# Performance work log

Hardware: AMD Instinct MI355X
Metric: run time of the kernel (lower is better)

The kernel has to match this reference:

```python
import jax, jax.numpy as jnp
import numpy as np

GOLDEN_CENTER = 1.0 / np.e
GOLDEN_LOWER = 0.5 - np.log(4.0 / 3.0)
GOLDEN_UPPER = 0.5


def setup_inputs() -> dict:
    key = jax.random.key(0)
    ks = jax.random.split(key, 5)
    B, T, D, E, F = 2, 2048, 2048, 8, 2048  # F = intermediate_size // (E//2) = 8192//4
    s_in = 1.0 / np.sqrt(D)
    s_f = 1.0 / np.sqrt(F)
    return {
        "x": jax.random.normal(ks[0], (B, T, D), dtype=jnp.float32),
        "Wg": jax.random.normal(ks[1], (E, D, F), dtype=jnp.float32) * s_in,
        "Wu": jax.random.normal(ks[2], (E, D, F), dtype=jnp.float32) * s_in,
        "Wd": jax.random.normal(ks[3], (E, F, D), dtype=jnp.float32) * s_f,
        "Wr": jax.random.normal(ks[4], (D, E), dtype=jnp.float32) * s_in,
        "temperature": jnp.ones((1,), dtype=jnp.float32),
    }


def _golden_weights(x, Wr, temperature):
    # router logits [B,T,E] -> sigmoid inhibition
    inh = jax.nn.sigmoid((x @ Wr) / temperature)
    in_zone = (inh >= GOLDEN_LOWER) & (inh <= GOLDEN_UPPER)
    distance = jnp.abs(inh - GOLDEN_CENTER)
    weights = jnp.exp(-distance / 0.1) * in_zone.astype(x.dtype)
    wsum = jnp.sum(weights, axis=-1, keepdims=True)
    no_expert = wsum < 1e-8
    # fallback: top-2 of a wider kernel (always computed; selected per-token via where)
    fb = jnp.exp(-distance / 0.3)
    _, top2 = jax.lax.top_k(fb, 2)  # [B,T,2]
    fb_mask = jnp.sum(jax.nn.one_hot(top2, weights.shape[-1], dtype=x.dtype), axis=-2)
    fb_w = fb * fb_mask
    fb_w = fb_w / jnp.maximum(jnp.sum(fb_w, axis=-1, keepdims=True), 1e-8)
    weights = jnp.where(no_expert, fb_w, weights)
    weights = weights / jnp.maximum(jnp.sum(weights, axis=-1, keepdims=True), 1e-8)
    return weights  # [B,T,E]


def reference(x, Wg, Wu, Wd, Wr, temperature):
    weights = _golden_weights(x, Wr, temperature)  # [B,T,E]
    gate = jnp.einsum("btd,edf->betf", x, Wg)
    up = jnp.einsum("btd,edf->betf", x, Wu)
    h = jax.nn.silu(gate) * up  # [B,E,T,F]
    e_out = jnp.einsum("betf,efd->betd", h, Wd)  # [B,E,T,D]
    out = jnp.einsum("bte,betd->btd", weights, e_out)
    return out
```

## Files before the change

### kernel.cpp

```cpp
#include <hip/hip_runtime.h>
#include <hip/hip_bf16.h>
#include <math.h>


#define E_NUM 8
#define BT_NUM 4096
#define MAT_ELEMS ((size_t)2048 * 2048)
#define MAXT 136

typedef short short8 __attribute__((ext_vector_type(8)));
typedef float f32x4 __attribute__((ext_vector_type(4)));
typedef __bf16 bf16x8 __attribute__((ext_vector_type(8)));

__device__ __forceinline__ short f2bf(float f) {
  __hip_bfloat16 h = __float2bfloat16(f);
  return __builtin_bit_cast(short, h);
}
__device__ __forceinline__ float bf2f(short s) {
  __hip_bfloat16 h = __builtin_bit_cast(__hip_bfloat16, s);
  return __bfloat162float(h);
}

#define GLOAD_LDS(gptr, lptr) \
  __builtin_amdgcn_global_load_lds( \
      (const __attribute__((address_space(1))) unsigned int*)(gptr), \
      (__attribute__((address_space(3))) unsigned int*)(lptr), 16, 0, 0)

#define LDS_OFF(p) ((unsigned)(size_t)(__attribute__((address_space(3))) const short*)(p))

#define DS_READ_B128(d, a) \
  asm volatile("ds_read_b128 %0, %1" : "=v"(d) : "v"(a))

#define BAR() __builtin_amdgcn_s_barrier()
#define LGKM0() do { \
  asm volatile("s_waitcnt lgkmcnt(0)" ::: "memory"); \
  __builtin_amdgcn_sched_barrier(0); \
} while (0)
#define VMC(n) asm volatile("s_waitcnt vmcnt(" #n ")" ::: "memory")

__global__ __launch_bounds__(256) void router_kernel(
    const float* __restrict__ x, const float* __restrict__ Wr,
    const float* __restrict__ temp, float* __restrict__ rw)
{
  const int bt = blockIdx.x;
  const int tid = threadIdx.x;
  const float* xp = x + (size_t)bt * 2048;
  float acc[E_NUM];
#pragma unroll
  for (int e = 0; e < E_NUM; e++) acc[e] = 0.f;
  for (int d = tid; d < 2048; d += 256) {
    float xv = xp[d];
    const float* wr = Wr + (size_t)d * E_NUM;
#pragma unroll
    for (int e = 0; e < E_NUM; e++) acc[e] += xv * wr[e];
  }
#pragma unroll
  for (int e = 0; e < E_NUM; e++) {
    float v = acc[e];
#pragma unroll
    for (int off = 32; off > 0; off >>= 1) v += __shfl_down(v, off, 64);
    acc[e] = v;
  }
  __shared__ float part[4][E_NUM];
  const int wid = tid >> 6, lane = tid & 63;
  if (lane == 0) {
#pragma unroll
    for (int e = 0; e < E_NUM; e++) part[wid][e] = acc[e];
  }
  __syncthreads();
  if (tid == 0) {
    const float t = temp[0];
    float wz[E_NUM], fb[E_NUM];
    float wsum = 0.f;
#pragma unroll
    for (int e = 0; e < E_NUM; e++) {
      float l = part[0][e] + part[1][e] + part[2][e] + part[3][e];
      float ih = 1.f / (1.f + expf(-l / t));
      float ds = fabsf(ih - 0.36787944117144233f);
      float in_zone = (ih >= 0.21231792754821915f && ih <= 0.5f) ? 1.f : 0.f;
      wz[e] = expf(-ds / 0.1f) * in_zone;
      wsum += wz[e];
      fb[e] = expf(-ds / 0.3f);
    }
    float w[E_NUM];
    if (wsum < 1e-8f) {
      int i1 = 0;
#pragma unroll
      for (int e = 1; e < E_NUM; e++) if (fb[e] > fb[i1]) i1 = e;
      int i2 = -1;
#pragma unroll
      for (int e = 0; e < E_NUM; e++) if (e != i1 && (i2 < 0 || fb[e] > fb[i2])) i2 = e;
      float s = fmaxf(fb[i1] + fb[i2], 1e-8f);
#pragma unroll
      for (int e = 0; e < E_NUM; e++) w[e] = (e == i1 || e == i2) ? fb[e] / s : 0.f;
    } else {
#pragma unroll
      for (int e = 0; e < E_NUM; e++) w[e] = wz[e];
    }
    float s2 = 0.f;
#pragma unroll
    for (int e = 0; e < E_NUM; e++) s2 += w[e];
    s2 = fmaxf(s2, 1e-8f);
    float inv = 1.f / s2;
#pragma unroll
    for (int e = 0; e < E_NUM; e++) rw[(size_t)bt * E_NUM + e] = w[e] * inv;
  }
}

__global__ void init_cnt_kernel(int* __restrict__ cnt) {
  if (threadIdx.x < 32) cnt[threadIdx.x] = 0;
}

__global__ __launch_bounds__(256) void build_idx_kernel(
    const float* __restrict__ rw, int* __restrict__ cnt,
    unsigned short* __restrict__ idx,
    unsigned short* __restrict__ inv, unsigned char* __restrict__ invn)
{
  const int t = blockIdx.x * 256 + threadIdx.x;
  const float* w = rw + (size_t)t * E_NUM;
  int s = 0;
#pragma unroll
  for (int e = 0; e < E_NUM; e++) {
    if (w[e] != 0.f) {
      int p = atomicAdd(&cnt[e], 1);
      idx[(size_t)e * BT_NUM + p] = (unsigned short)t;
      inv[(size_t)t * E_NUM + s] = (unsigned short)((e << 12) | p);
      s++;
    }
  }
  invn[t] = (unsigned char)s;
}

__global__ void pack_tiles_kernel(int* __restrict__ cnt) {
  if (threadIdx.x == 0) {
    int n = 0;
    for (int e = 0; e < E_NUM; e++) {
      const int nt = (cnt[e] + 255) >> 8;
      for (int by = 0; by < nt; by++) cnt[32 + n++] = (e << 8) | by;
    }
    cnt[16] = n;
  }
}

__global__ __launch_bounds__(256) void zero_out_kernel(float* __restrict__ out) {
  const size_t i = ((size_t)blockIdx.x * 256 + threadIdx.x) * 4;
  *(f32x4*)(out + i) = (f32x4){0.f, 0.f, 0.f, 0.f};
}

__global__ __launch_bounds__(256) void cvt_x_kernel(
    const float* __restrict__ x, short* __restrict__ xb)
{
  const size_t base = ((size_t)blockIdx.x * 256 + threadIdx.x) * 8;
  f32x4 v0 = *(const f32x4*)(x + base);
  f32x4 v1 = *(const f32x4*)(x + base + 4);
  short8 p;
#pragma unroll
  for (int j = 0; j < 4; j++) { p[j] = f2bf(v0[j]); p[4 + j] = f2bf(v1[j]); }
  *(short8*)(xb + base) = p;
}

__global__ __launch_bounds__(256) void transpose_cvt_kernel(
    const float* __restrict__ sg, const float* __restrict__ su, const float* __restrict__ sd,
    short* __restrict__ dgu, short* __restrict__ dd, int nexp)
{
  const int which = blockIdx.z / nexp, e = blockIdx.z % nexp;
  __shared__ float t[32][33];
  const int tx = threadIdx.x, ty = threadIdx.y;
  const int x0 = blockIdx.x * 32, y0 = blockIdx.y * 32;
  const float* s = (which == 0 ? sg : which == 1 ? su : sd) + (size_t)e * MAT_ELEMS;
#pragma unroll
  for (int i = ty; i < 32; i += 8) t[i][tx] = s[(size_t)(y0 + i) * 2048 + x0 + tx];
  __syncthreads();
  if (which < 2) {
    short* d = dgu + (size_t)e * (2 * MAT_ELEMS);
#pragma unroll
    for (int i = ty; i < 32; i += 8) {
      const int col = x0 + i;
      const int np = ((col >> 5) * 64) + which * 32 + (col & 31);
      d[(size_t)np * 2048 + y0 + tx] = f2bf(t[tx][i]);
    }
  } else {
#pragma unroll
    for (int i = ty; i < 32; i += 8)
      dd[(size_t)e * MAT_ELEMS + (size_t)(x0 + i) * 2048 + y0 + tx] = f2bf(t[tx][i]);
  }
}

__device__ __forceinline__ void gemm_core8(
    const short* a00, const short* a01, const short* a10, const short* a11,
    const short* __restrict__ Bb, const int T,
    short* As, short* Bs, f32x4 (&acc)[8][4])
{
  const int tid = threadIdx.x;
  const int w = tid >> 6, lane = tid & 63;
  const int wm = w >> 2, wn = w & 3;
  const int r = lane & 15, g4 = lane >> 4;
  const int l3 = lane >> 3, l7 = lane & 7;

  const size_t bOff = (size_t)(w * 16 + l3) * 2048 + (size_t)((l7 ^ l3) * 8);
  const int wdst = w * 1024;

  const unsigned aB = LDS_OFF(As), bB = LDS_OFF(Bs);
  unsigned aro[2][4], bro[2][2], csb[2];
#pragma unroll
  for (int mh = 0; mh < 2; mh++)
#pragma unroll
    for (int mq = 0; mq < 4; mq++)
      aro[mh][mq] = aB + (unsigned)(wm * 16384 + (mh * 64 + mq * 16 + r) * 128);
#pragma unroll
  for (int nh = 0; nh < 2; nh++)
#pragma unroll
    for (int nq = 0; nq < 2; nq++) {
      const int row = wn * 64 + nh * 32 + nq * 16 + r;
      bro[nh][nq] = bB + (unsigned)((row >> 7) * 16384 + (row & 127) * 128);
    }
#pragma unroll
  for (int kk = 0; kk < 2; kk++)
    csb[kk] = (unsigned)((((kk * 4 + g4) ^ (r & 7)) * 16));

#pragma unroll
  for (int i = 0; i < 8; i++)
#pragma unroll
    for (int jn = 0; jn < 4; jn++) acc[i][jn] = (f32x4){0.f, 0.f, 0.f, 0.f};

#define STG_A(tt, hh) do { \
  const short* g0_ = ((hh) ? a10 : a00) + (tt) * 64; \
  const short* g1_ = ((hh) ? a11 : a01) + (tt) * 64; \
  short* ld_ = As + ((tt) & 1) * 16384 + (hh) * 8192 + wdst; \
  GLOAD_LDS(g0_, ld_); GLOAD_LDS(g1_, ld_ + 512); \
} while (0)

#define STG_B(tt, hh) do { \
  const short* g_ = Bb + bOff + (size_t)(hh) * 128 * 2048 + (tt) * 64; \
  short* ld_ = Bs + ((tt) & 1) * 16384 + (hh) * 8192 + wdst; \
  GLOAD_LDS(g_, ld_); GLOAD_LDS(g_ + (size_t)8 * 2048, ld_ + 512); \
} while (0)

#define RD_A(mh, b32) do { \
  _Pragma("unroll") \
  for (int mq = 0; mq < 4; mq++) \
    _Pragma("unroll") \
    for (int kk = 0; kk < 2; kk++) \
      DS_READ_B128(Ar[mq * 2 + kk], aro[mh][mq] + (b32) + csb[kk]); \
} while (0)

#define RD_B(nh, DST, b32) do { \
  _Pragma("unroll") \
  for (int nq = 0; nq < 2; nq++) \
    _Pragma("unroll") \
    for (int kk = 0; kk < 2; kk++) \
      DS_READ_B128(DST[nq * 2 + kk], bro[nh][nq] + (b32) + csb[kk]); \
} while (0)

#define MM(BV, mh, nh) do { \
  __builtin_amdgcn_s_setprio(1); \
  _Pragma("unroll") \
  for (int kk = 0; kk < 2; kk++) \
    _Pragma("unroll") \
    for (int mq = 0; mq < 4; mq++) \
      _Pragma("unroll") \
      for (int nq = 0; nq < 2; nq++) \
        acc[(mh) * 4 + mq][(nh) * 2 + nq] = \
            __builtin_amdgcn_mfma_f32_16x16x32_bf16( \
                __builtin_bit_cast(bf16x8, Ar[mq * 2 + kk]), \
                __builtin_bit_cast(bf16x8, BV[nq * 2 + kk]), \
                acc[(mh) * 4 + mq][(nh) * 2 + nq], 0, 0, 0); \
  __builtin_amdgcn_s_setprio(0); \
} while (0)

  STG_B(0, 0); STG_B(0, 1);
  STG_A(0, 0); STG_A(0, 1);
  STG_B(1, 0); STG_B(1, 1);
  VMC(4);
  BAR();

  short8 Ar[8], B0[4], B1[4];

  for (int t = 0; t < T; t += 2) {
    const int t1 = t + 1;
    const int t2 = (t + 2 < T) ? t + 2 : 0;
    const int t3 = (t + 3 < T) ? t + 3 : 1;
    RD_A(0, 0u); RD_B(0, B0, 0u);
    STG_A(t1, 0);
    BAR(); LGKM0(); MM(B0, 0, 0); BAR();
    RD_B(1, B1, 0u);
    STG_A(t1, 1);
    BAR(); LGKM0(); MM(B1, 0, 1); BAR();
    RD_A(1, 0u);
    STG_B(t2, 0);
    BAR(); LGKM0(); MM(B0, 1, 0); BAR();
    STG_B(t2, 1);
    BAR(); MM(B1, 1, 1);
    VMC(4);
    BAR();
    RD_A(0, 32768u); RD_B(0, B0, 32768u);
    STG_A(t2, 0);
    BAR(); LGKM0(); MM(B0, 0, 0); BAR();
    RD_B(1, B1, 32768u);
    STG_A(t2, 1);
    BAR(); LGKM0(); MM(B1, 0, 1); BAR();
    RD_A(1, 32768u);
    STG_B(t3, 0);
    BAR(); LGKM0(); MM(B0, 1, 0); BAR();
    STG_B(t3, 1);
    BAR(); MM(B1, 1, 1);
    VMC(4);
    BAR();
  }
  VMC(0);
#undef STG_A
#undef STG_B
#undef RD_A
#undef RD_B
#undef MM
  __builtin_amdgcn_sched_barrier(0);
  asm volatile("s_nop 7\n\ts_nop 7" ::: "memory");
}

__global__ __launch_bounds__(512, 1) void fused_gu_kernel(
    const short* __restrict__ xb, const short* __restrict__ Bgu,
    short* __restrict__ h, const float* __restrict__ rw,
    const unsigned short* __restrict__ idx, const int* __restrict__ cnt,
    int e_param, int packed)
{
  int e, by, eb;
  if (packed) {
    const int nt = cnt[16];
    if ((int)blockIdx.y >= nt) return;
    const int tl = cnt[32 + blockIdx.y];
    e = tl >> 8; by = tl & 255; eb = e;
  } else {
    e = e_param; by = blockIdx.y; eb = 0;
  }
  const int cntE = cnt[e];
  const int m0 = by * 256;
  if (m0 >= cntE) return;
  const int bx = blockIdx.x;
  const int n0 = bx * 256;
  const unsigned short* idxe = idx + (size_t)e * BT_NUM;

  __shared__ short As_[32768];
  __shared__ short Bs_[32768];

  const int tid = threadIdx.x;
  const int w = tid >> 6, lane = tid & 63;
  const int l3 = lane >> 3, l7 = lane & 7;
  const int r0 = m0 + w * 16 + l3;
  const int cm = cntE - 1;
  const size_t swz = (size_t)((l7 ^ l3) * 8);
  const short* a00 = xb + (size_t)idxe[min(r0, cm)] * 2048 + swz;
  const short* a01 = xb + (size_t)idxe[min(r0 + 8, cm)] * 2048 + swz;
  const short* a10 = xb + (size_t)idxe[min(r0 + 128, cm)] * 2048 + swz;
  const short* a11 = xb + (size_t)idxe[min(r0 + 136, cm)] * 2048 + swz;

  f32x4 acc[8][4];
  gemm_core8(a00, a01, a10, a11,
             Bgu + (size_t)eb * (2 * MAT_ELEMS) + (size_t)n0 * 2048,
             32, As_, Bs_, acc);

  short* he = h + (size_t)eb * BT_NUM * 2048;
  const int wm = w >> 2, wn = w & 3;
  const int rr = lane & 15, g4 = lane >> 4;
#pragma unroll
  for (int mi = 0; mi < 8; mi++) {
#pragma unroll
    for (int j = 0; j < 4; j++) {
      const int row = m0 + wm * 128 + (mi >> 2) * 64 + (mi & 3) * 16 + g4 * 4 + j;
      const int tok = idxe[min(row, cm)];
      const float wt = rw[(size_t)tok * 8 + e];
#pragma unroll
      for (int nq = 0; nq < 2; nq++) {
        const float g = acc[mi][nq][j];
        const float u = acc[mi][2 + nq][j];
        const float hv = (g / (1.f + __expf(-g))) * u * wt;
        const int c = (bx * 4 + wn) * 32 + nq * 16 + rr;
        he[(size_t)row * 2048 + c] = f2bf(hv);
      }
    }
  }
}

__global__ __launch_bounds__(512, 1) void down_kernel(
    const short* __restrict__ h, const short* __restrict__ WdT,
    short* __restrict__ dout, const int* __restrict__ cnt)
{
  const int nt = cnt[16];
  if ((int)blockIdx.y >= nt) return;
  const int tl = cnt[32 + blockIdx.y];
  const int e = tl >> 8, by = tl & 255;
  const int cntE = cnt[e];
  const int m0 = by * 256;
  if (m0 >= cntE) return;
  const int bx = blockIdx.x;
  const int n0 = bx * 256;

  __shared__ short As_[32768];
  __shared__ short Bs_[32768];

  const int tid = threadIdx.x;
  const int w = tid >> 6, lane = tid & 63;
  const int l3 = lane >> 3, l7 = lane & 7;
  const size_t swz = (size_t)((l7 ^ l3) * 8);
  const short* he = h + (size_t)e * BT_NUM * 2048;
  const short* a00 = he + (size_t)(m0 + w * 16 + l3) * 2048 + swz;
  const short* a01 = a00 + (size_t)8 * 2048;
  const short* a10 = a00 + (size_t)128 * 2048;
  const short* a11 = a00 + (size_t)136 * 2048;

  f32x4 acc[8][4];
  gemm_core8(a00, a01, a10, a11,
             WdT + (size_t)e * MAT_ELEMS + (size_t)n0 * 2048,
             32, As_, Bs_, acc);

  short* de = dout + (size_t)e * BT_NUM * 2048;
  const int wm = w >> 2, wn = w & 3;
  const int rr = lane & 15, g4 = lane >> 4;
#pragma unroll
  for (int mi = 0; mi < 8; mi++) {
#pragma unroll
    for (int ni = 0; ni < 4; ni++) {
      const int col = n0 + wn * 64 + (ni >> 1) * 32 + (ni & 1) * 16 + rr;
#pragma unroll
      for (int j = 0; j < 4; j++) {
        const int row = m0 + wm * 128 + (mi >> 2) * 64 + (mi & 3) * 16 + g4 * 4 + j;
        de[(size_t)row * 2048 + col] = f2bf(acc[mi][ni][j]);
      }
    }
  }
}

__global__ __launch_bounds__(512, 1) void down_atomic_kernel(
    const short* __restrict__ h, const short* __restrict__ WdT,
    float* __restrict__ out,
    const unsigned short* __restrict__ idx, const int* __restrict__ cnt,
    int e_param)
{
  const int e = e_param;
  const int cntE = cnt[e];
  const int by = blockIdx.y, bx = blockIdx.x;
  const int m0 = by * 256;
  if (m0 >= cntE) return;
  const int n0 = bx * 256;
  const unsigned short* idxe = idx + (size_t)e * BT_NUM;

  __shared__ short As_[32768];
  __shared__ short Bs_[32768];

  const int tid = threadIdx.x;
  const int w = tid >> 6, lane = tid & 63;
  const int l3 = lane >> 3, l7 = lane & 7;
  const size_t swz = (size_t)((l7 ^ l3) * 8);
  const short* a00 = h + (size_t)(m0 + w * 16 + l3) * 2048 + swz;
  const short* a01 = a00 + (size_t)8 * 2048;
  const short* a10 = a00 + (size_t)128 * 2048;
  const short* a11 = a00 + (size_t)136 * 2048;

  f32x4 acc[8][4];
  gemm_core8(a00, a01, a10, a11, WdT + (size_t)n0 * 2048, 32, As_, Bs_, acc);

  const int wm = w >> 2, wn = w & 3;
  const int rr = lane & 15, g4 = lane >> 4;
#pragma unroll
  for (int mi = 0; mi < 8; mi++) {
#pragma unroll
    for (int ni = 0; ni < 4; ni++) {
      const int col = n0 + wn * 64 + (ni >> 1) * 32 + (ni & 1) * 16 + rr;
#pragma unroll
      for (int j = 0; j < 4; j++) {
        const int row = m0 + wm * 128 + (mi >> 2) * 64 + (mi & 3) * 16 + g4 * 4 + j;
        if (row < cntE) {
          const int tok = idxe[row];
          unsafeAtomicAdd(&out[(size_t)tok * 2048 + col], acc[mi][ni][j]);
        }
      }
    }
  }
}

__global__ __launch_bounds__(256) void combine_kernel(
    const short* __restrict__ dout, const unsigned short* __restrict__ inv,
    const unsigned char* __restrict__ invn, float* __restrict__ out)
{
  const int t = blockIdx.x;
  const int nv = invn[t];
  const int c = threadIdx.x * 8;
  float s[8];
#pragma unroll
  for (int j = 0; j < 8; j++) s[j] = 0.f;
  for (int v = 0; v < nv; v++) {
    const unsigned entry = inv[(size_t)t * E_NUM + v];
    const size_t rowoff = ((size_t)(entry >> 12) * BT_NUM + (entry & 4095)) * 2048;
    const short8 d8 = *(const short8*)&dout[rowoff + c];
#pragma unroll
    for (int j = 0; j < 8; j++) s[j] += bf2f(d8[j]);
  }
  float* op = out + (size_t)t * 2048 + c;
  *(f32x4*)op = (f32x4){s[0], s[1], s[2], s[3]};
  *(f32x4*)(op + 4) = (f32x4){s[4], s[5], s[6], s[7]};
}

extern "C" void kernel_launch(void* const* d_in, const int* in_sizes, int n_in,
                              void* d_out, int out_size, void* d_ws, size_t ws_size,
                              hipStream_t stream)
{
  const float* x  = (const float*)d_in[0];
  const float* Wg = (const float*)d_in[1];
  const float* Wu = (const float*)d_in[2];
  const float* Wd = (const float*)d_in[3];
  const float* Wr = (const float*)d_in[4];
  const float* tp = (const float*)d_in[5];
  float* out = (float*)d_out;

  char* ws = (char*)d_ws;
  const size_t SZ_RW   = 131072;
  const size_t SZ_CNT  = 4096;
  const size_t SZ_IDX  = (size_t)E_NUM * BT_NUM * 2;
  const size_t SZ_INV  = (size_t)BT_NUM * E_NUM * 2;
  const size_t SZ_INVN = 8192;
  const size_t SZ_XB   = (size_t)BT_NUM * 2048 * 2;
  const size_t SZ_BGU_E = 2 * MAT_ELEMS * 2;
  const size_t SZ_WDT_E = MAT_ELEMS * 2;
  const size_t SZ_H_E  = (size_t)BT_NUM * 2048 * 2;

  const size_t HEAD = SZ_RW + SZ_CNT + SZ_IDX + SZ_INV + SZ_INVN;
  const size_t FULL = HEAD + SZ_XB + 8 * SZ_BGU_E + 8 * SZ_WDT_E + 8 * SZ_H_E;

  float* rw = (float*)ws;
  int* cnt = (int*)(ws + SZ_RW);
  unsigned short* idx = (unsigned short*)(ws + SZ_RW + SZ_CNT);
  unsigned short* inv = (unsigned short*)(ws + SZ_RW + SZ_CNT + SZ_IDX);
  unsigned char* invn = (unsigned char*)(ws + SZ_RW + SZ_CNT + SZ_IDX + SZ_INV);
  short* xb = (short*)(ws + HEAD);
  char* rest = ws + HEAD + SZ_XB;

  router_kernel<<<BT_NUM, 256, 0, stream>>>(x, Wr, tp, rw);
  init_cnt_kernel<<<1, 64, 0, stream>>>(cnt);
  build_idx_kernel<<<16, 256, 0, stream>>>(rw, cnt, idx, inv, invn);
  pack_tiles_kernel<<<1, 64, 0, stream>>>(cnt);
  cvt_x_kernel<<<4096, 256, 0, stream>>>(x, xb);

  if (ws_size >= FULL) {
    short* Bgu = (short*)rest;
    short* WdT = (short*)(rest + 8 * SZ_BGU_E);
    short* h   = (short*)(rest + 8 * SZ_BGU_E + 8 * SZ_WDT_E);
    short* dout = Bgu;

    transpose_cvt_kernel<<<dim3(64, 64, 24), dim3(32, 8), 0, stream>>>(
        Wg, Wu, Wd, Bgu, WdT, 8);
    fused_gu_kernel<<<dim3(16, MAXT), 512, 0, stream>>>(
        xb, Bgu, h, rw, idx, cnt, 0, 1);
    down_kernel<<<dim3(8, MAXT), 512, 0, stream>>>(h, WdT, dout, cnt);
    combine_kernel<<<BT_NUM, 256, 0, stream>>>(dout, inv, invn, out);
  } else {
    short* Bgu = (short*)rest;
    short* WdT = (short*)(rest + SZ_BGU_E);
    short* h   = (short*)(rest + SZ_BGU_E + SZ_WDT_E);

    zero_out_kernel<<<8192, 256, 0, stream>>>(out);
    for (int e = 0; e < 8; e++) {
      transpose_cvt_kernel<<<dim3(64, 64, 3), dim3(32, 8), 0, stream>>>(
          Wg + (size_t)e * MAT_ELEMS, Wu + (size_t)e * MAT_ELEMS,
          Wd + (size_t)e * MAT_ELEMS, Bgu, WdT, 1);
      fused_gu_kernel<<<dim3(16, 16), 512, 0, stream>>>(
          xb, Bgu, h, rw, idx, cnt, e, 0);
      down_atomic_kernel<<<dim3(8, 16), 512, 0, stream>>>(
          h, WdT, out, idx, cnt, e);
    }
  }
}
```

Measured before the change: 674.1 us.

## Remap GEMM tiles per XCD and widen transpose tiles with packed bf16 stores

The grouped GEMM kernels now linearize the block index and remap it so that consecutive logical tiles, which share the same expert and row block, land on the same XCD. This is meant to improve L2 reuse of the shared A rows and B weight columns across the chiplets. Separately, the weight transpose/convert kernel now handles 32x64 tiles and writes two bf16 values per store, halving the grid and widening writes. The remap assumes round-robin dispatch of blocks across 8 XCDs, and the LDS tile changes shape and padding.

```diff
diff --git a/kernel.cpp b/kernel.cpp
--- a/kernel.cpp
+++ b/kernel.cpp
@@ -9,6 +9,7 @@
 #define MAXT 136
 
 typedef short short8 __attribute__((ext_vector_type(8)));
+typedef short short2v __attribute__((ext_vector_type(2)));
 typedef float f32x4 __attribute__((ext_vector_type(4)));
 typedef __bf16 bf16x8 __attribute__((ext_vector_type(8)));
 
@@ -37,6 +38,13 @@
   __builtin_amdgcn_sched_barrier(0); \
 } while (0)
 #define VMC(n) asm volatile("s_waitcnt vmcnt(" #n ")" ::: "memory")
+
+__device__ __forceinline__ int xcd_unmap(int o, int nact) {
+  const int q = nact >> 3, rr = nact & 7;
+  const int xcd = o & 7, seq = o >> 3;
+  return (xcd < rr) ? xcd * (q + 1) + seq
+                    : rr * (q + 1) + (xcd - rr) * q + seq;
+}
 
 __global__ __launch_bounds__(256) void router_kernel(
     const float* __restrict__ x, const float* __restrict__ Wr,
@@ -164,25 +172,31 @@
     short* __restrict__ dgu, short* __restrict__ dd, int nexp)
 {
   const int which = blockIdx.z / nexp, e = blockIdx.z % nexp;
-  __shared__ float t[32][33];
+  __shared__ float t[32][65];
   const int tx = threadIdx.x, ty = threadIdx.y;
-  const int x0 = blockIdx.x * 32, y0 = blockIdx.y * 32;
+  const int x0 = blockIdx.x * 32, y0 = blockIdx.y * 64;
   const float* s = (which == 0 ? sg : which == 1 ? su : sd) + (size_t)e * MAT_ELEMS;
 #pragma unroll
-  for (int i = ty; i < 32; i += 8) t[i][tx] = s[(size_t)(y0 + i) * 2048 + x0 + tx];
+  for (int i = 0; i < 8; i++)
+    t[tx][ty + 8 * i] = s[(size_t)(y0 + ty + 8 * i) * 2048 + x0 + tx];
   __syncthreads();
   if (which < 2) {
     short* d = dgu + (size_t)e * (2 * MAT_ELEMS);
 #pragma unroll
-    for (int i = ty; i < 32; i += 8) {
-      const int col = x0 + i;
+    for (int i = 0; i < 4; i++) {
+      const int row = ty + 8 * i;
+      const int col = x0 + row;
       const int np = ((col >> 5) * 64) + which * 32 + (col & 31);
-      d[(size_t)np * 2048 + y0 + tx] = f2bf(t[tx][i]);
+      short2v v = {f2bf(t[row][2 * tx]), f2bf(t[row][2 * tx + 1])};
+      *(short2v*)&d[(size_t)np * 2048 + y0 + 2 * tx] = v;
     }
   } else {
 #pragma unroll
-    for (int i = ty; i < 32; i += 8)
-      dd[(size_t)e * MAT_ELEMS + (size_t)(x0 + i) * 2048 + y0 + tx] = f2bf(t[tx][i]);
+    for (int i = 0; i < 4; i++) {
+      const int row = ty + 8 * i;
+      short2v v = {f2bf(t[row][2 * tx]), f2bf(t[row][2 * tx + 1])};
+      *(short2v*)&dd[(size_t)e * MAT_ELEMS + (size_t)(x0 + row) * 2048 + y0 + 2 * tx] = v;
+    }
   }
 }
 
@@ -323,19 +337,21 @@
     const unsigned short* __restrict__ idx, const int* __restrict__ cnt,
     int e_param, int packed)
 {
-  int e, by, eb;
+  int e, by, bx, eb;
   if (packed) {
     const int nt = cnt[16];
-    if ((int)blockIdx.y >= nt) return;
-    const int tl = cnt[32 + blockIdx.y];
-    e = tl >> 8; by = tl & 255; eb = e;
+    const int nact = nt * 16;
+    const int o = blockIdx.y * 16 + blockIdx.x;
+    if (o >= nact) return;
+    const int l = xcd_unmap(o, nact);
+    const int tl = cnt[32 + (l >> 4)];
+    e = tl >> 8; by = tl & 255; bx = l & 15; eb = e;
   } else {
-    e = e_param; by = blockIdx.y; eb = 0;
+    e = e_param; by = blockIdx.y; bx = blockIdx.x; eb = 0;
   }
   const int cntE = cnt[e];
   const int m0 = by * 256;
   if (m0 >= cntE) return;
-  const int bx = blockIdx.x;
   const int n0 = bx * 256;
   const unsigned short* idxe = idx + (size_t)e * BT_NUM;
 
@@ -385,13 +401,15 @@
     short* __restrict__ dout, const int* __restrict__ cnt)
 {
   const int nt = cnt[16];
-  if ((int)blockIdx.y >= nt) return;
-  const int tl = cnt[32 + blockIdx.y];
-  const int e = tl >> 8, by = tl & 255;
+  const int nact = nt * 8;
+  const int o = blockIdx.y * 8 + blockIdx.x;
+  if (o >= nact) return;
+  const int l = xcd_unmap(o, nact);
+  const int tl = cnt[32 + (l >> 3)];
+  const int e = tl >> 8, by = tl & 255, bx = l & 7;
   const int cntE = cnt[e];
   const int m0 = by * 256;
   if (m0 >= cntE) return;
-  const int bx = blockIdx.x;
   const int n0 = bx * 256;
 
   __shared__ short As_[32768];
@@ -545,7 +563,7 @@
     short* h   = (short*)(rest + 8 * SZ_BGU_E + 8 * SZ_WDT_E);
     short* dout = Bgu;
 
-    transpose_cvt_kernel<<<dim3(64, 64, 24), dim3(32, 8), 0, stream>>>(
+    transpose_cvt_kernel<<<dim3(64, 32, 24), dim3(32, 8), 0, stream>>>(
         Wg, Wu, Wd, Bgu, WdT, 8);
     fused_gu_kernel<<<dim3(16, MAXT), 512, 0, stream>>>(
         xb, Bgu, h, rw, idx, cnt, 0, 1);
@@ -558,7 +576,7 @@
 
     zero_out_kernel<<<8192, 256, 0, stream>>>(out);
     for (int e = 0; e < 8; e++) {
-      transpose_cvt_kernel<<<dim3(64, 64, 3), dim3(32, 8), 0, stream>>>(
+      transpose_cvt_kernel<<<dim3(64, 32, 3), dim3(32, 8), 0, stream>>>(
           Wg + (size_t)e * MAT_ELEMS, Wu + (size_t)e * MAT_ELEMS,
           Wd + (size_t)e * MAT_ELEMS, Bgu, WdT, 1);
       fused_gu_kernel<<<dim3(16, 16), 512, 0, stream>>>(
```

New measurement: 612.8 us. -9.1%, faster.
